# Optimization experiments

Measured on AMD Instinct MI355X. Metric: run time of the kernel, lower is better.

The kernel has to match this reference:

```python
import jax, jax.numpy as jnp
import numpy as np

N_ANCH = 8400      # YOLOv8 anchors for 640x640
NUM_CLS = 600
H_IMG = 640
W_IMG = 640
PRE_NMS = 1024     # fixed pre-NMS pool (replaces dynamic NMS input size)
M_MAX = 31         # fixed max surviving detections (padded)
OUT = 224
SCORE_THRESH = 0.1
IOU_THRESH = 0.45
SCALES = jnp.array([0.7071, 1.0, 1.4142], jnp.float32)
MEAN = jnp.array([0.485, 0.456, 0.406], jnp.float32).reshape(1, 3, 1, 1)
STD = jnp.array([0.229, 0.224, 0.225], jnp.float32).reshape(1, 3, 1, 1)
ALLOWED = [41, 68, 70, 74, 87, 95, 113, 144, 150, 158, 164, 165, 193, 205, 212, 224,
           257, 298, 310, 335, 351, 354, 390, 393, 401, 403, 439, 442, 457, 466, 489,
           510, 512, 514, 524, 530, 531, 543, 546, 554, 565, 573, 580, 587, 588, 591]


def setup_inputs() -> dict:
    key = jax.random.key(0)
    k1, k2, k3, k4 = jax.random.split(key, 4)
    # box channels: cx,cy in pixel coords; w,h in [20, 200] px
    cxcy = jax.random.uniform(k1, (1, 2, N_ANCH), jnp.float32) * jnp.array([W_IMG, H_IMG], jnp.float32).reshape(1, 2, 1)
    wh = jax.random.uniform(k2, (1, 2, N_ANCH), jnp.float32) * 180.0 + 20.0
    logits = jax.random.uniform(k3, (1, NUM_CLS, N_ANCH), jnp.float32)
    raw_pred = jnp.concatenate([cxcy, wh, logits], axis=1)
    image = jax.random.uniform(k4, (1, 3, H_IMG, W_IMG), jnp.float32)
    allowed_cl = jnp.array(ALLOWED, jnp.int32)
    return {"raw_pred": raw_pred, "image": image, "allowed_cl": allowed_cl}


def _pairwise_iou(b):
    # b: [P,4] (x1,y1,x2,y2) -> [P,P] IoU (torchvision convention, no +1)
    area = (b[:, 2] - b[:, 0]) * (b[:, 3] - b[:, 1])
    lt = jnp.maximum(b[:, None, :2], b[None, :, :2])   # [P,P,2]
    rb = jnp.minimum(b[:, None, 2:], b[None, :, 2:])
    wh = jnp.clip(rb - lt, 0.0)
    inter = wh[..., 0] * wh[..., 1]
    union = area[:, None] + area[None, :] - inter
    return inter / jnp.maximum(union, 1e-12)


def _greedy_nms(iou, thr):
    # boxes assumed pre-sorted by descending score
    n = iou.shape[0]
    rng = jnp.arange(n)

    def step(supp, i):
        keep_i = jnp.logical_not(supp[i])
        supp = supp | (keep_i & (iou[i] > thr) & (rng > i))
        return supp, keep_i

    _, keep = jax.lax.scan(step, jnp.zeros(n, bool), rng)
    return keep


def _crop_bilinear(img, box):
    # img: [3,H,W]; box: (x1,y1,x2,y2). roi_align, aligned=True, sampling_ratio=1.
    C, H, W = img.shape
    x1, y1, x2, y2 = box[0], box[1], box[2], box[3]
    bw = (x2 - x1) / OUT
    bh = (y2 - y1) / OUT
    r = jnp.arange(OUT, dtype=jnp.float32) + 0.5
    xs = x1 - 0.5 + r * bw
    ys = y1 - 0.5 + r * bh
    mx = (xs > -1.0) & (xs < W)
    my = (ys > -1.0) & (ys < H)
    xsc = jnp.clip(xs, 0.0, W - 1.0)
    ysc = jnp.clip(ys, 0.0, H - 1.0)
    y0 = jnp.floor(ysc).astype(jnp.int32)
    x0 = jnp.floor(xsc).astype(jnp.int32)
    y1i = jnp.minimum(y0 + 1, H - 1)
    x1i = jnp.minimum(x0 + 1, W - 1)
    wy = ysc - y0.astype(jnp.float32)
    wx = xsc - x0.astype(jnp.float32)
    # separable bilinear: interp rows along y, then columns along x
    rows = img[:, y0, :] * (1.0 - wy)[None, :, None] + img[:, y1i, :] * wy[None, :, None]  # [3,OUT,W]
    out = rows[:, :, x0] * (1.0 - wx)[None, None, :] + rows[:, :, x1i] * wx[None, None, :]  # [3,OUT,OUT]
    return out * (my[None, :, None] & mx[None, None, :]).astype(img.dtype)


def reference(raw_pred, image, allowed_cl):
    x = raw_pred[0].T                            # [N, 4+C]
    cx, cy, w, h = x[:, 0], x[:, 1], x[:, 2], x[:, 3]
    boxes = jnp.stack([cx - w * 0.5, cy - h * 0.5, cx + w * 0.5, cy + h * 0.5], axis=1)
    logits = x[:, 4:]
    scores = logits.max(axis=1)
    classes = logits.argmax(axis=1).astype(jnp.int32)

    # fixed-size pre-NMS pool, sorted by descending score
    sc, idx = jax.lax.top_k(scores, PRE_NMS)
    b = boxes[idx]
    cl = classes[idx]

    keep = _greedy_nms(_pairwise_iou(b), IOU_THRESH)
    in_allowed = (cl[:, None] == allowed_cl[None, :].astype(cl.dtype)).any(axis=1)
    valid = keep & (sc > SCORE_THRESH) & in_allowed

    masked = jnp.where(valid, sc, -jnp.inf)
    topv, topi = jax.lax.top_k(masked, M_MAX)
    sel_valid = topv > -jnp.inf
    sel_boxes = jnp.where(sel_valid[:, None], b[topi], 0.0)
    sel_scores = jnp.where(sel_valid, sc[topi], 0.0)
    sel_cls = jnp.where(sel_valid, cl[topi], 0)

    full_box = jnp.array([[0.0, 0.0, W_IMG - 1.0, H_IMG - 1.0]], jnp.float32)
    final_boxes = jnp.concatenate([full_box, sel_boxes], axis=0)            # [M+1,4]
    final_scores = jnp.concatenate([jnp.ones((1,), jnp.float32), sel_scores])
    final_classes = jnp.concatenate([-jnp.ones((1,), cl.dtype), sel_cls])

    # multi-scale boxes, same center, clamped to image
    bx1, by1, bx2, by2 = (final_boxes[:, i] for i in range(4))
    ccx = (bx1 + bx2) * 0.5
    ccy = (by1 + by2) * 0.5
    ww = (bx2 - bx1)[:, None] * SCALES[None, :] * 0.5
    hh = (by2 - by1)[:, None] * SCALES[None, :] * 0.5
    scaled = jnp.stack([
        jnp.clip(ccx[:, None] - ww, 0.0, W_IMG - 1.0),
        jnp.clip(ccy[:, None] - hh, 0.0, H_IMG - 1.0),
        jnp.clip(ccx[:, None] + ww, 0.0, W_IMG - 1.0),
        jnp.clip(ccy[:, None] + hh, 0.0, H_IMG - 1.0),
    ], axis=-1)                                                             # [M+1,K,4]

    boxes_flat = scaled.reshape(-1, 4)                                      # [(M+1)*K,4]
    crops = jax.vmap(lambda bb: _crop_bilinear(image[0], bb))(boxes_flat)   # [(M+1)*K,3,224,224]
    crops_norm = (crops - MEAN) / STD
    return final_boxes, final_scores, final_classes, crops_norm
```

## Files before the change

### kernel.cpp

```cpp
#include <hip/hip_runtime.h>
#include <hip/hip_bf16.h>
#include <stdint.h>

#define N_ANCH   8400
#define NUM_CLS  600
#define H_IMG    640
#define W_IMG    640
#define PRE_NMS  1024
#define M_MAX    31
#define OUT_SZ   224
#define SCORE_THRESH 0.1f
#define IOU_THRESH   0.45f

__global__ __launch_bounds__(512) void k_prep(
    const float* __restrict__ raw,
    float* __restrict__ x1, float* __restrict__ y1,
    float* __restrict__ x2, float* __restrict__ y2,
    float* __restrict__ sc, int* __restrict__ cls) {
  __shared__ float s_m[8][64];
  __shared__ int   s_mi[8][64];
  const int lane = threadIdx.x & 63;
  const int part = threadIdx.x >> 6;
  const int a = blockIdx.x * 64 + lane;

  float m = -INFINITY; int mi = 0;
  if (a < N_ANCH) {
    const float* lp = raw + (size_t)(4 + part * 75) * N_ANCH + a;
    #pragma unroll 5
    for (int cc = 0; cc < 75; ++cc) {
      float v = lp[(size_t)cc * N_ANCH];
      if (v > m) { m = v; mi = part * 75 + cc; }
    }
  }
  s_m[part][lane] = m; s_mi[part][lane] = mi;
  __syncthreads();
  if (part == 0 && a < N_ANCH) {
    #pragma unroll
    for (int p = 1; p < 8; ++p) {
      float vm = s_m[p][lane];
      if (vm > m) { m = vm; mi = s_mi[p][lane]; }
    }
    sc[a] = m; cls[a] = mi;
    float cx = raw[a];
    float cy = raw[(size_t)1 * N_ANCH + a];
    float w  = raw[(size_t)2 * N_ANCH + a];
    float h  = raw[(size_t)3 * N_ANCH + a];
    x1[a] = cx - w * 0.5f; y1[a] = cy - h * 0.5f;
    x2[a] = cx + w * 0.5f; y2[a] = cy + h * 0.5f;
  }
}

__device__ __forceinline__ unsigned long long shflxor64(unsigned long long v, int j) {
  int lo = __shfl_xor((int)(unsigned int)v, j, 64);
  int hi = __shfl_xor((int)(unsigned int)(v >> 32), j, 64);
  return ((unsigned long long)(unsigned int)hi << 32) | (unsigned int)lo;
}

__global__ __launch_bounds__(1024) void k_select(
    const float* __restrict__ sc, const int* __restrict__ cls,
    const float* __restrict__ x1, const float* __restrict__ y1,
    const float* __restrict__ x2, const float* __restrict__ y2,
    float* __restrict__ t_sc, float* __restrict__ tb, int* __restrict__ t_cl) {
  __shared__ unsigned int hist[8][2048];
  __shared__ unsigned long long C[N_ANCH];
  __shared__ unsigned long long s_sel[PRE_NMS];
  __shared__ unsigned int wt[16];
  __shared__ int s_bstar, s_above, s_cnt;
  __shared__ unsigned long long s_thr;

  const int tid = threadIdx.x;
  const int lane = tid & 63, wid = tid >> 6;
  unsigned int* hf = &hist[0][0];

  unsigned long long ka[9];
  bool kv[9];
  #pragma unroll
  for (int e = 0; e < 9; ++e) {
    int a = tid + e * 1024;
    kv[e] = (a < N_ANCH);
    float s = kv[e] ? sc[a] : 0.0f;
    ka[e] = (((unsigned long long)__float_as_uint(s)) << 32) |
            (unsigned long long)(0xFFFFFFFFu - (unsigned)a);
  }

  int need = PRE_NMS;
  unsigned long long thr = 0ULL;
  int m = 0;

  #pragma unroll
  for (int i = tid; i < 8 * 2048; i += 1024) hf[i] = 0;
  if (tid == 0) s_cnt = 0;
  __syncthreads();
  #pragma unroll
  for (int e = 0; e < 9; ++e)
    if (kv[e]) atomicAdd(&hist[wid & 7][(unsigned)((ka[e] >> 51) & 2047ULL)], 1u);
  __syncthreads();
  {
    unsigned int h0 = 0, h1 = 0;
    #pragma unroll
    for (int cp = 0; cp < 8; ++cp) { h0 += hist[cp][2 * tid]; h1 += hist[cp][2 * tid + 1]; }
    unsigned int suf = h0 + h1;
    #pragma unroll
    for (int o = 1; o < 64; o <<= 1) {
      unsigned int t = __shfl_down(suf, o, 64);
      if (lane + o < 64) suf += t;
    }
    if (lane == 0) wt[wid] = suf;
    __syncthreads();
    unsigned int add = 0;
    #pragma unroll
    for (int q = 0; q < 16; ++q) if (q > wid) add += wt[q];
    const unsigned int S0 = suf + add, S1 = S0 - h0, S2 = S1 - h1;
    if ((int)S0 >= need && (int)S1 < need) { s_bstar = 2 * tid;     s_above = (int)S1; }
    if ((int)S1 >= need && (int)S2 < need) { s_bstar = 2 * tid + 1; s_above = (int)S2; }
  }
  __syncthreads();
  {
    const int bstar = s_bstar;
    need -= s_above;
    thr |= (unsigned long long)bstar << 51;
    #pragma unroll
    for (int e = 0; e < 9; ++e)
      if (kv[e] && (int)((ka[e] >> 51) & 2047ULL) == bstar)
        C[atomicAdd(&s_cnt, 1)] = ka[e];
  }
  __syncthreads();
  m = s_cnt;

  const int shifts[5] = {40, 29, 18, 7, 0};
  for (int si = 0; si < 5 && m > 64; ++si) {
    const int shift = shifts[si];
    unsigned long long cu[9];
    #pragma unroll
    for (int e = 0; e < 9; ++e) {
      int i = tid + e * 1024;
      cu[e] = (i < m) ? C[i] : 0ULL;
    }
    #pragma unroll
    for (int i = tid; i < 8 * 2048; i += 1024) hf[i] = 0;
    if (tid == 0) s_cnt = 0;
    __syncthreads();
    #pragma unroll
    for (int e = 0; e < 9; ++e)
      if (tid + e * 1024 < m)
        atomicAdd(&hist[wid & 7][(unsigned)((cu[e] >> shift) & 2047ULL)], 1u);
    __syncthreads();
    {
      unsigned int h0 = 0, h1 = 0;
      #pragma unroll
      for (int cp = 0; cp < 8; ++cp) { h0 += hist[cp][2 * tid]; h1 += hist[cp][2 * tid + 1]; }
      unsigned int suf = h0 + h1;
      #pragma unroll
      for (int o = 1; o < 64; o <<= 1) {
        unsigned int t = __shfl_down(suf, o, 64);
        if (lane + o < 64) suf += t;
      }
      if (lane == 0) wt[wid] = suf;
      __syncthreads();
      unsigned int add = 0;
      #pragma unroll
      for (int q = 0; q < 16; ++q) if (q > wid) add += wt[q];
      const unsigned int S0 = suf + add, S1 = S0 - h0, S2 = S1 - h1;
      if ((int)S0 >= need && (int)S1 < need) { s_bstar = 2 * tid;     s_above = (int)S1; }
      if ((int)S1 >= need && (int)S2 < need) { s_bstar = 2 * tid + 1; s_above = (int)S2; }
    }
    __syncthreads();
    {
      const int bstar = s_bstar;
      need -= s_above;
      thr |= (unsigned long long)bstar << shift;
      #pragma unroll
      for (int e = 0; e < 9; ++e)
        if (tid + e * 1024 < m && (int)((cu[e] >> shift) & 2047ULL) == bstar)
          C[atomicAdd(&s_cnt, 1)] = cu[e];
    }
    __syncthreads();
    m = s_cnt;
  }

  if (wid == 0) {
    unsigned long long v = (lane < m) ? C[lane] : 0ULL;
    for (int k2 = 2; k2 <= 64; k2 <<= 1) {
      for (int j = k2 >> 1; j > 0; j >>= 1) {
        unsigned long long pv = shflxor64(v, j);
        bool keepmax = (((lane & k2) == 0) == ((lane & j) == 0));
        if (keepmax == (pv > v)) v = pv;
      }
    }
    if (lane == need - 1) s_thr = v;
  }
  if (tid == 0) s_cnt = 0;
  __syncthreads();

  const unsigned long long thrv = s_thr;
  #pragma unroll
  for (int e = 0; e < 9; ++e)
    if (kv[e] && ka[e] >= thrv) {
      int p = atomicAdd(&s_cnt, 1);
      if (p < PRE_NMS) s_sel[p] = ka[e];
    }
  __syncthreads();

  unsigned long long v = s_sel[tid];
  for (int k2 = 2; k2 <= PRE_NMS; k2 <<= 1) {
    for (int j = k2 >> 1; j > 0; j >>= 1) {
      unsigned long long pv;
      if (j >= 64) {
        __syncthreads();
        C[tid] = v;
        __syncthreads();
        pv = C[tid ^ j];
      } else {
        pv = shflxor64(v, j);
      }
      bool keepmax = (((tid & k2) == 0) == ((tid & j) == 0));
      if (keepmax == (pv > v)) v = pv;
    }
  }

  const int idx = (int)(0xFFFFFFFFu - (unsigned)(v & 0xFFFFFFFFULL));
  t_sc[tid] = __uint_as_float((unsigned)(v >> 32));
  tb[tid]               = x1[idx];
  tb[PRE_NMS + tid]     = y1[idx];
  tb[2 * PRE_NMS + tid] = x2[idx];
  tb[3 * PRE_NMS + tid] = y2[idx];
  t_cl[tid] = cls[idx];
}

__global__ __launch_bounds__(256) void k_iou_mask(
    const float* __restrict__ tb, unsigned long long* __restrict__ mask) {
  __shared__ float bx1[PRE_NMS], by1[PRE_NMS], bx2[PRE_NMS], by2[PRE_NMS], bar[PRE_NMS];
  const int tid = threadIdx.x;
  for (int a = tid; a < PRE_NMS; a += 256) {
    float X1 = tb[a], Y1 = tb[PRE_NMS + a], X2 = tb[2 * PRE_NMS + a], Y2 = tb[3 * PRE_NMS + a];
    bx1[a] = X1; by1[a] = Y1; bx2[a] = X2; by2[a] = Y2;
    bar[a] = (X2 - X1) * (Y2 - Y1);
  }
  __syncthreads();
  const int g = blockIdx.x * 256 + tid;
  const int i = g >> 4;
  const int w = g & 15;
  const float ix1 = bx1[i], iy1 = by1[i], ix2 = bx2[i], iy2 = by2[i], ia = bar[i];
  unsigned long long m = 0ULL;
  const int j0 = w * 64;
  #pragma unroll 8
  for (int l = 0; l < 64; ++l) {
    const int jj = (l + 4 * w) & 63;
    const int j = j0 + jj;
    float ltx = fmaxf(ix1, bx1[j]);
    float lty = fmaxf(iy1, by1[j]);
    float rbx = fminf(ix2, bx2[j]);
    float rby = fminf(iy2, by2[j]);
    float ww = fmaxf(rbx - ltx, 0.0f);
    float hh = fmaxf(rby - lty, 0.0f);
    float inter = ww * hh;
    float uni = ia + bar[j] - inter;
    float iou = inter / fmaxf(uni, 1e-12f);
    if (iou > IOU_THRESH && j > i) m |= (1ULL << jj);
  }
  mask[(size_t)i * 16 + w] = m;
}

__device__ __forceinline__ unsigned long long rdlane64(unsigned long long v, int lane) {
  unsigned int lo = (unsigned int)v;
  unsigned int hi = (unsigned int)(v >> 32);
  unsigned int a = (unsigned int)__builtin_amdgcn_readlane((int)lo, lane);
  unsigned int b = (unsigned int)__builtin_amdgcn_readlane((int)hi, lane);
  return ((unsigned long long)b << 32) | (unsigned long long)a;
}

__global__ __launch_bounds__(1024) void k_nms_final(
    const unsigned long long* __restrict__ mask,
    const float* __restrict__ t_sc, const float* __restrict__ tb,
    const int* __restrict__ t_cl, const int* __restrict__ allowed, int n_allowed,
    float* __restrict__ out, float* __restrict__ cropbox) {
  __shared__ unsigned long long L[PRE_NMS * 17];
  __shared__ unsigned long long s_K[16];
  __shared__ unsigned long long s_albm[16];
  __shared__ int s_selr[M_MAX];
  __shared__ int s_nsel;
  const int tid = threadIdx.x;
  const int lane = tid & 63, wid = tid >> 6;

  const ulonglong2* m2 = (const ulonglong2*)mask;
  #pragma unroll
  for (int k = 0; k < 8; ++k) {
    int t2 = tid + k * 1024;
    ulonglong2 val = m2[t2];
    int row = t2 >> 3;
    int w0 = (t2 & 7) * 2;
    L[row * 17 + w0]     = val.x;
    L[row * 17 + w0 + 1] = val.y;
  }
  if (tid < 16) s_albm[tid] = 0ULL;
  __syncthreads();
  if (tid < n_allowed) {
    int c = allowed[tid];
    atomicOr(&s_albm[c >> 6], 1ULL << (c & 63));
  }

  unsigned long long suppw = 0ULL;

  for (int c = 0; c < 16; ++c) {
    if (wid == c) {
      unsigned long long d = L[(c * 64 + lane) * 17 + c];
      unsigned int slo = (unsigned int)__builtin_amdgcn_readfirstlane((int)(unsigned int)suppw);
      unsigned int shi = (unsigned int)__builtin_amdgcn_readfirstlane((int)(unsigned int)(suppw >> 32));
      unsigned long long sup = ((unsigned long long)shi << 32) | slo;
      unsigned long long K = 0ULL;
      #pragma unroll
      for (int i = 0; i < 64; ++i) {
        unsigned long long di = rdlane64(d, i);
        const bool kept = ((sup >> i) & 1ULL) == 0ULL;
        K   |= kept ? (1ULL << i) : 0ULL;
        sup |= kept ? di : 0ULL;
      }
      if (lane == 0) s_K[c] = K;
    }
    __syncthreads();
    {
      unsigned long long Kc = s_K[c];
      unsigned long long v =
          ((Kc >> (unsigned)lane) & 1ULL) ? L[(c * 64 + lane) * 17 + wid] : 0ULL;
      #pragma unroll
      for (int o = 1; o < 64; o <<= 1) v |= shflxor64(v, o);
      suppw |= v;
    }
  }
  __syncthreads();

  if (wid == 0) {
    bool validf[16];
    int cnt = 0;
    #pragma unroll
    for (int k = 0; k < 16; ++k) {
      const int r = lane * 16 + k;
      bool kp = ((s_K[r >> 6] >> (unsigned)(r & 63)) & 1ULL) != 0ULL;
      float s = t_sc[r];
      int c = t_cl[r];
      bool ina = ((s_albm[c >> 6] >> (unsigned)(c & 63)) & 1ULL) != 0ULL;
      bool v = kp && (s > SCORE_THRESH) && ina;
      validf[k] = v;
      cnt += v ? 1 : 0;
    }
    int scan = cnt;
    #pragma unroll
    for (int o = 1; o < 64; o <<= 1) {
      int v = __shfl_up(scan, o, 64);
      if (lane >= o) scan += v;
    }
    const int excl = scan - cnt;
    int rk = excl;
    #pragma unroll
    for (int k = 0; k < 16; ++k) {
      if (validf[k]) {
        if (rk < M_MAX) s_selr[rk] = lane * 16 + k;
        rk++;
      }
    }
    if (lane == 63) s_nsel = (scan < M_MAX) ? scan : M_MAX;
  }
  __syncthreads();

  if (wid == 0 && lane < 32) {
    const int nsel = s_nsel;
    float b0, b1, b2, b3, fsc, fcl;
    if (lane == 0) {
      b0 = 0.0f; b1 = 0.0f; b2 = (float)(W_IMG - 1); b3 = (float)(H_IMG - 1);
      fsc = 1.0f; fcl = -1.0f;
    } else if (lane <= nsel) {
      int r = s_selr[lane - 1];
      b0 = tb[r]; b1 = tb[PRE_NMS + r]; b2 = tb[2 * PRE_NMS + r]; b3 = tb[3 * PRE_NMS + r];
      fsc = t_sc[r]; fcl = (float)t_cl[r];
    } else {
      b0 = b1 = b2 = b3 = 0.0f; fsc = 0.0f; fcl = 0.0f;
    }
    out[lane * 4 + 0] = b0; out[lane * 4 + 1] = b1;
    out[lane * 4 + 2] = b2; out[lane * 4 + 3] = b3;
    out[128 + lane] = fsc;
    out[160 + lane] = fcl;

    const float ccx = (b0 + b2) * 0.5f;
    const float ccy = (b1 + b3) * 0.5f;
    const float bwd = b2 - b0;
    const float bhd = b3 - b1;
    const float scl3[3] = {0.7071f, 1.0f, 1.4142f};
    #pragma unroll
    for (int s3 = 0; s3 < 3; ++s3) {
      float ww = bwd * scl3[s3] * 0.5f;
      float hh = bhd * scl3[s3] * 0.5f;
      float cx1 = fminf(fmaxf(ccx - ww, 0.0f), (float)(W_IMG - 1));
      float cy1 = fminf(fmaxf(ccy - hh, 0.0f), (float)(H_IMG - 1));
      float cx2 = fminf(fmaxf(ccx + ww, 0.0f), (float)(W_IMG - 1));
      float cy2 = fminf(fmaxf(ccy + hh, 0.0f), (float)(H_IMG - 1));
      const int bi = (lane * 3 + s3) * 4;
      cropbox[bi + 0] = cx1; cropbox[bi + 1] = cy1;
      cropbox[bi + 2] = cx2; cropbox[bi + 3] = cy2;
    }
  }
}

__global__ __launch_bounds__(256) void k_crop(
    const float* __restrict__ img, const float* __restrict__ cropbox,
    float* __restrict__ out) {
  const int gid = blockIdx.x * 256 + threadIdx.x;
  const int x4 = gid % (OUT_SZ / 4);
  const int t1 = gid / (OUT_SZ / 4);
  const int py = t1 % OUT_SZ;
  const int t2 = t1 / OUT_SZ;
  const int c = t2 % 3;
  const int b = t2 / 3;
  if (b >= 96) return;

  const float bx1 = cropbox[b * 4 + 0];
  const float by1 = cropbox[b * 4 + 1];
  const float bx2 = cropbox[b * 4 + 2];
  const float by2 = cropbox[b * 4 + 3];
  const float bw = (bx2 - bx1) / (float)OUT_SZ;
  const float bh = (by2 - by1) / (float)OUT_SZ;

  const float ys = by1 - 0.5f + ((float)py + 0.5f) * bh;
  const bool my = (ys > -1.0f) && (ys < (float)H_IMG);
  const float ysc = fminf(fmaxf(ys, 0.0f), (float)(H_IMG - 1));
  const int y0 = (int)floorf(ysc);
  const int y1i = min(y0 + 1, H_IMG - 1);
  const float wy = ysc - (float)y0;

  const float* r0p = img + (size_t)c * (H_IMG * W_IMG) + (size_t)y0 * W_IMG;
  const float* r1p = img + (size_t)c * (H_IMG * W_IMG) + (size_t)y1i * W_IMG;

  const float mean = (c == 0) ? 0.485f : ((c == 1) ? 0.456f : 0.406f);
  const float stdv = (c == 0) ? 0.229f : ((c == 1) ? 0.224f : 0.225f);

  auto pix = [&](int px) -> float {
    const float xs = bx1 - 0.5f + ((float)px + 0.5f) * bw;
    const bool mx = (xs > -1.0f) && (xs < (float)W_IMG);
    const float xsc = fminf(fmaxf(xs, 0.0f), (float)(W_IMG - 1));
    const int x0 = (int)floorf(xsc);
    const int x1i = min(x0 + 1, W_IMG - 1);
    const float wx = xsc - (float)x0;
    const float r0 = r0p[x0] * (1.0f - wy) + r1p[x0] * wy;
    const float r1 = r0p[x1i] * (1.0f - wy) + r1p[x1i] * wy;
    float v = r0 * (1.0f - wx) + r1 * wx;
    v = (mx && my) ? v : 0.0f;
    return (v - mean) / stdv;
  };

  const int pxb = x4 * 4;
  float4 res;
  res.x = pix(pxb + 0);
  res.y = pix(pxb + 1);
  res.z = pix(pxb + 2);
  res.w = pix(pxb + 3);
  reinterpret_cast<float4*>(out)[gid] = res;
}

extern "C" void kernel_launch(void* const* d_in, const int* in_sizes, int n_in,
                              void* d_out, int out_size, void* d_ws, size_t ws_size,
                              hipStream_t stream) {
  const float* raw = (const float*)d_in[0];
  const float* img = (const float*)d_in[1];
  const int* allowed = (const int*)d_in[2];
  float* out = (float*)d_out;

  unsigned long long* mask = (unsigned long long*)d_ws;
  float* fbase = (float*)((char*)d_ws + (size_t)PRE_NMS * 16 * 8);
  float* x1 = fbase + 0 * N_ANCH;
  float* y1 = fbase + 1 * N_ANCH;
  float* x2 = fbase + 2 * N_ANCH;
  float* y2 = fbase + 3 * N_ANCH;
  float* sc = fbase + 4 * N_ANCH;
  int*   cls = (int*)(fbase + 5 * N_ANCH);
  float* t_sc = fbase + 6 * N_ANCH;
  float* tb   = t_sc + PRE_NMS;
  int*   t_cl = (int*)(tb + 4 * PRE_NMS);
  float* cropbox = (float*)(t_cl + PRE_NMS);

  k_prep<<<(N_ANCH + 63) / 64, 512, 0, stream>>>(raw, x1, y1, x2, y2, sc, cls);
  k_select<<<1, 1024, 0, stream>>>(sc, cls, x1, y1, x2, y2, t_sc, tb, t_cl);
  k_iou_mask<<<64, 256, 0, stream>>>(tb, mask);
  k_nms_final<<<1, 1024, 0, stream>>>(mask, t_sc, tb, t_cl, allowed,
                                      in_sizes[2], out, cropbox);
  const int total4 = 96 * 3 * OUT_SZ * OUT_SZ / 4;
  k_crop<<<(total4 + 255) / 256, 256, 0, stream>>>(img, cropbox, out + 192);
}
```

Measured before the change: 130.2 us.

## Transpose IoU mask layout and stream NMS columns from global memory into registers

New measurement: 128.5 us. Within noise of the previous version (-1.3%).

```diff
diff --git a/kernel.cpp b/kernel.cpp
--- a/kernel.cpp
+++ b/kernel.cpp
@@ -228,7 +228,7 @@
 }
 
 __global__ __launch_bounds__(256) void k_iou_mask(
-    const float* __restrict__ tb, unsigned long long* __restrict__ mask) {
+    const float* __restrict__ tb, unsigned long long* __restrict__ maskT) {
   __shared__ float bx1[PRE_NMS], by1[PRE_NMS], bx2[PRE_NMS], by2[PRE_NMS], bar[PRE_NMS];
   const int tid = threadIdx.x;
   for (int a = tid; a < PRE_NMS; a += 256) {
@@ -238,14 +238,13 @@
   }
   __syncthreads();
   const int g = blockIdx.x * 256 + tid;
-  const int i = g >> 4;
-  const int w = g & 15;
+  const int w = g >> 10;
+  const int i = g & 1023;
   const float ix1 = bx1[i], iy1 = by1[i], ix2 = bx2[i], iy2 = by2[i], ia = bar[i];
   unsigned long long m = 0ULL;
   const int j0 = w * 64;
   #pragma unroll 8
-  for (int l = 0; l < 64; ++l) {
-    const int jj = (l + 4 * w) & 63;
+  for (int jj = 0; jj < 64; ++jj) {
     const int j = j0 + jj;
     float ltx = fmaxf(ix1, bx1[j]);
     float lty = fmaxf(iy1, by1[j]);
@@ -258,7 +257,7 @@
     float iou = inter / fmaxf(uni, 1e-12f);
     if (iou > IOU_THRESH && j > i) m |= (1ULL << jj);
   }
-  mask[(size_t)i * 16 + w] = m;
+  maskT[g] = m;
 }
 
 __device__ __forceinline__ unsigned long long rdlane64(unsigned long long v, int lane) {
@@ -270,11 +269,10 @@
 }
 
 __global__ __launch_bounds__(1024) void k_nms_final(
-    const unsigned long long* __restrict__ mask,
+    const unsigned long long* __restrict__ maskT,
     const float* __restrict__ t_sc, const float* __restrict__ tb,
     const int* __restrict__ t_cl, const int* __restrict__ allowed, int n_allowed,
     float* __restrict__ out, float* __restrict__ cropbox) {
-  __shared__ unsigned long long L[PRE_NMS * 17];
   __shared__ unsigned long long s_K[16];
   __shared__ unsigned long long s_albm[16];
   __shared__ int s_selr[M_MAX];
@@ -282,16 +280,6 @@
   const int tid = threadIdx.x;
   const int lane = tid & 63, wid = tid >> 6;
 
-  const ulonglong2* m2 = (const ulonglong2*)mask;
-  #pragma unroll
-  for (int k = 0; k < 8; ++k) {
-    int t2 = tid + k * 1024;
-    ulonglong2 val = m2[t2];
-    int row = t2 >> 3;
-    int w0 = (t2 & 7) * 2;
-    L[row * 17 + w0]     = val.x;
-    L[row * 17 + w0 + 1] = val.y;
-  }
   if (tid < 16) s_albm[tid] = 0ULL;
   __syncthreads();
   if (tid < n_allowed) {
@@ -299,34 +287,50 @@
     atomicOr(&s_albm[c >> 6], 1ULL << (c & 63));
   }
 
+  const unsigned long long* colbase = maskT + (size_t)wid * 1024;
   unsigned long long suppw = 0ULL;
 
-  for (int c = 0; c < 16; ++c) {
-    if (wid == c) {
-      unsigned long long d = L[(c * 64 + lane) * 17 + c];
-      unsigned int slo = (unsigned int)__builtin_amdgcn_readfirstlane((int)(unsigned int)suppw);
-      unsigned int shi = (unsigned int)__builtin_amdgcn_readfirstlane((int)(unsigned int)(suppw >> 32));
-      unsigned long long sup = ((unsigned long long)shi << 32) | slo;
-      unsigned long long K = 0ULL;
-      #pragma unroll
-      for (int i = 0; i < 64; ++i) {
-        unsigned long long di = rdlane64(d, i);
-        const bool kept = ((sup >> i) & 1ULL) == 0ULL;
-        K   |= kept ? (1ULL << i) : 0ULL;
-        sup |= kept ? di : 0ULL;
-      }
-      if (lane == 0) s_K[c] = K;
-    }
-    __syncthreads();
-    {
-      unsigned long long Kc = s_K[c];
-      unsigned long long v =
-          ((Kc >> (unsigned)lane) & 1ULL) ? L[(c * 64 + lane) * 17 + wid] : 0ULL;
-      #pragma unroll
-      for (int o = 1; o < 64; o <<= 1) v |= shflxor64(v, o);
-      suppw |= v;
-    }
-  }
+  unsigned long long rA = colbase[lane];
+  unsigned long long rB = colbase[64 + lane];
+
+#define NMS_STEP(REG, CHUNK)                                                  \
+  {                                                                           \
+    if (wid == (CHUNK)) {                                                     \
+      unsigned int slo = (unsigned int)__builtin_amdgcn_readfirstlane(        \
+          (int)(unsigned int)suppw);                                          \
+      unsigned int shi = (unsigned int)__builtin_amdgcn_readfirstlane(        \
+          (int)(unsigned int)(suppw >> 32));                                  \
+      unsigned long long sup = ((unsigned long long)shi << 32) | slo;         \
+      unsigned long long K = 0ULL;                                            \
+      _Pragma("unroll")                                                       \
+      for (int i = 0; i < 64; ++i) {                                          \
+        unsigned long long di = rdlane64((REG), i);                           \
+        const bool kept = ((sup >> i) & 1ULL) == 0ULL;                        \
+        K   |= kept ? (1ULL << i) : 0ULL;                                     \
+        sup |= kept ? di : 0ULL;                                              \
+      }                                                                       \
+      if (lane == 0) s_K[(CHUNK)] = K;                                        \
+    }                                                                         \
+    __syncthreads();                                                          \
+    {                                                                         \
+      unsigned long long Kc = s_K[(CHUNK)];                                   \
+      unsigned long long v =                                                  \
+          ((Kc >> (unsigned)lane) & 1ULL) ? (REG) : 0ULL;                     \
+      _Pragma("unroll")                                                       \
+      for (int o = 1; o < 64; o <<= 1) v |= shflxor64(v, o);                  \
+      suppw |= v;                                                             \
+    }                                                                         \
+  }
+
+  #pragma unroll 1
+  for (int c = 0; c < 16; c += 2) {
+    unsigned long long nA = (c + 2 < 16) ? colbase[(c + 2) * 64 + lane] : 0ULL;
+    NMS_STEP(rA, c)
+    unsigned long long nB = (c + 3 < 16) ? colbase[(c + 3) * 64 + lane] : 0ULL;
+    NMS_STEP(rB, c + 1)
+    rA = nA; rB = nB;
+  }
+#undef NMS_STEP
   __syncthreads();
 
   if (wid == 0) {
@@ -463,7 +467,7 @@
   const int* allowed = (const int*)d_in[2];
   float* out = (float*)d_out;
 
-  unsigned long long* mask = (unsigned long long*)d_ws;
+  unsigned long long* maskT = (unsigned long long*)d_ws;
   float* fbase = (float*)((char*)d_ws + (size_t)PRE_NMS * 16 * 8);
   float* x1 = fbase + 0 * N_ANCH;
   float* y1 = fbase + 1 * N_ANCH;
@@ -478,8 +482,8 @@
 
   k_prep<<<(N_ANCH + 63) / 64, 512, 0, stream>>>(raw, x1, y1, x2, y2, sc, cls);
   k_select<<<1, 1024, 0, stream>>>(sc, cls, x1, y1, x2, y2, t_sc, tb, t_cl);
-  k_iou_mask<<<64, 256, 0, stream>>>(tb, mask);
-  k_nms_final<<<1, 1024, 0, stream>>>(mask, t_sc, tb, t_cl, allowed,
+  k_iou_mask<<<64, 256, 0, stream>>>(tb, maskT);
+  k_nms_final<<<1, 1024, 0, stream>>>(maskT, t_sc, tb, t_cl, allowed,
                                       in_sizes[2], out, cropbox);
   const int total4 = 96 * 3 * OUT_SZ * OUT_SZ / 4;
   k_crop<<<(total4 + 255) / 256, 256, 0, stream>>>(img, cropbox, out + 192);
```

## Fuse IoU mask computation into single-block NMS kernel with triangular work balance

Applied to the files above, without the earlier changes.

Measured after the change: 227.7 us. +74.8%, slower.

```diff
diff --git a/kernel.cpp b/kernel.cpp
--- a/kernel.cpp
+++ b/kernel.cpp
@@ -227,40 +227,6 @@
   t_cl[tid] = cls[idx];
 }
 
-__global__ __launch_bounds__(256) void k_iou_mask(
-    const float* __restrict__ tb, unsigned long long* __restrict__ mask) {
-  __shared__ float bx1[PRE_NMS], by1[PRE_NMS], bx2[PRE_NMS], by2[PRE_NMS], bar[PRE_NMS];
-  const int tid = threadIdx.x;
-  for (int a = tid; a < PRE_NMS; a += 256) {
-    float X1 = tb[a], Y1 = tb[PRE_NMS + a], X2 = tb[2 * PRE_NMS + a], Y2 = tb[3 * PRE_NMS + a];
-    bx1[a] = X1; by1[a] = Y1; bx2[a] = X2; by2[a] = Y2;
-    bar[a] = (X2 - X1) * (Y2 - Y1);
-  }
-  __syncthreads();
-  const int g = blockIdx.x * 256 + tid;
-  const int i = g >> 4;
-  const int w = g & 15;
-  const float ix1 = bx1[i], iy1 = by1[i], ix2 = bx2[i], iy2 = by2[i], ia = bar[i];
-  unsigned long long m = 0ULL;
-  const int j0 = w * 64;
-  #pragma unroll 8
-  for (int l = 0; l < 64; ++l) {
-    const int jj = (l + 4 * w) & 63;
-    const int j = j0 + jj;
-    float ltx = fmaxf(ix1, bx1[j]);
-    float lty = fmaxf(iy1, by1[j]);
-    float rbx = fminf(ix2, bx2[j]);
-    float rby = fminf(iy2, by2[j]);
-    float ww = fmaxf(rbx - ltx, 0.0f);
-    float hh = fmaxf(rby - lty, 0.0f);
-    float inter = ww * hh;
-    float uni = ia + bar[j] - inter;
-    float iou = inter / fmaxf(uni, 1e-12f);
-    if (iou > IOU_THRESH && j > i) m |= (1ULL << jj);
-  }
-  mask[(size_t)i * 16 + w] = m;
-}
-
 __device__ __forceinline__ unsigned long long rdlane64(unsigned long long v, int lane) {
   unsigned int lo = (unsigned int)v;
   unsigned int hi = (unsigned int)(v >> 32);
@@ -269,12 +235,12 @@
   return ((unsigned long long)b << 32) | (unsigned long long)a;
 }
 
-__global__ __launch_bounds__(1024) void k_nms_final(
-    const unsigned long long* __restrict__ mask,
+__global__ __launch_bounds__(1024) void k_iou_nms(
     const float* __restrict__ t_sc, const float* __restrict__ tb,
     const int* __restrict__ t_cl, const int* __restrict__ allowed, int n_allowed,
     float* __restrict__ out, float* __restrict__ cropbox) {
-  __shared__ unsigned long long L[PRE_NMS * 17];
+  __shared__ unsigned long long L[16 * PRE_NMS];
+  __shared__ float bx1[PRE_NMS], by1[PRE_NMS], bx2[PRE_NMS], by2[PRE_NMS], bar[PRE_NMS];
   __shared__ unsigned long long s_K[16];
   __shared__ unsigned long long s_albm[16];
   __shared__ int s_selr[M_MAX];
@@ -282,15 +248,11 @@
   const int tid = threadIdx.x;
   const int lane = tid & 63, wid = tid >> 6;
 
-  const ulonglong2* m2 = (const ulonglong2*)mask;
-  #pragma unroll
-  for (int k = 0; k < 8; ++k) {
-    int t2 = tid + k * 1024;
-    ulonglong2 val = m2[t2];
-    int row = t2 >> 3;
-    int w0 = (t2 & 7) * 2;
-    L[row * 17 + w0]     = val.x;
-    L[row * 17 + w0 + 1] = val.y;
+  {
+    float X1 = tb[tid], Y1 = tb[PRE_NMS + tid];
+    float X2 = tb[2 * PRE_NMS + tid], Y2 = tb[3 * PRE_NMS + tid];
+    bx1[tid] = X1; by1[tid] = Y1; bx2[tid] = X2; by2[tid] = Y2;
+    bar[tid] = (X2 - X1) * (Y2 - Y1);
   }
   if (tid < 16) s_albm[tid] = 0ULL;
   __syncthreads();
@@ -299,11 +261,40 @@
     atomicOr(&s_albm[c >> 6], 1ULL << (c & 63));
   }
 
+  {
+    const int g = wid >> 2, r = wid & 3;
+    const int q = (g == 0) ? r : (g == 1) ? (15 - r) : (g == 2) ? (4 + r) : (11 - r);
+    const int i = q * 64 + lane;
+    const float ix1 = bx1[i], iy1 = by1[i], ix2 = bx2[i], iy2 = by2[i], ia = bar[i];
+    for (int k = 0; k < 16; ++k) {
+      unsigned long long m = 0ULL;
+      if (k >= q) {
+        const int j0 = k * 64;
+        #pragma unroll 8
+        for (int jj = 0; jj < 64; ++jj) {
+          const int j = j0 + jj;
+          float ltx = fmaxf(ix1, bx1[j]);
+          float lty = fmaxf(iy1, by1[j]);
+          float rbx = fminf(ix2, bx2[j]);
+          float rby = fminf(iy2, by2[j]);
+          float ww = fmaxf(rbx - ltx, 0.0f);
+          float hh = fmaxf(rby - lty, 0.0f);
+          float inter = ww * hh;
+          float uni = ia + bar[j] - inter;
+          float iou = inter / fmaxf(uni, 1e-12f);
+          if (iou > IOU_THRESH && j > i) m |= (1ULL << jj);
+        }
+      }
+      L[k * PRE_NMS + i] = m;
+    }
+  }
+  __syncthreads();
+
   unsigned long long suppw = 0ULL;
-
+  #pragma unroll 1
   for (int c = 0; c < 16; ++c) {
     if (wid == c) {
-      unsigned long long d = L[(c * 64 + lane) * 17 + c];
+      unsigned long long d = L[c * PRE_NMS + c * 64 + lane];
       unsigned int slo = (unsigned int)__builtin_amdgcn_readfirstlane((int)(unsigned int)suppw);
       unsigned int shi = (unsigned int)__builtin_amdgcn_readfirstlane((int)(unsigned int)(suppw >> 32));
       unsigned long long sup = ((unsigned long long)shi << 32) | slo;
@@ -321,7 +312,7 @@
     {
       unsigned long long Kc = s_K[c];
       unsigned long long v =
-          ((Kc >> (unsigned)lane) & 1ULL) ? L[(c * 64 + lane) * 17 + wid] : 0ULL;
+          ((Kc >> (unsigned)lane) & 1ULL) ? L[wid * PRE_NMS + c * 64 + lane] : 0ULL;
       #pragma unroll
       for (int o = 1; o < 64; o <<= 1) v |= shflxor64(v, o);
       suppw |= v;
@@ -370,7 +361,7 @@
       fsc = 1.0f; fcl = -1.0f;
     } else if (lane <= nsel) {
       int r = s_selr[lane - 1];
-      b0 = tb[r]; b1 = tb[PRE_NMS + r]; b2 = tb[2 * PRE_NMS + r]; b3 = tb[3 * PRE_NMS + r];
+      b0 = bx1[r]; b1 = by1[r]; b2 = bx2[r]; b3 = by2[r];
       fsc = t_sc[r]; fcl = (float)t_cl[r];
     } else {
       b0 = b1 = b2 = b3 = 0.0f; fsc = 0.0f; fcl = 0.0f;
@@ -463,7 +454,6 @@
   const int* allowed = (const int*)d_in[2];
   float* out = (float*)d_out;
 
-  unsigned long long* mask = (unsigned long long*)d_ws;
   float* fbase = (float*)((char*)d_ws + (size_t)PRE_NMS * 16 * 8);
   float* x1 = fbase + 0 * N_ANCH;
   float* y1 = fbase + 1 * N_ANCH;
@@ -478,9 +468,8 @@
 
   k_prep<<<(N_ANCH + 63) / 64, 512, 0, stream>>>(raw, x1, y1, x2, y2, sc, cls);
   k_select<<<1, 1024, 0, stream>>>(sc, cls, x1, y1, x2, y2, t_sc, tb, t_cl);
-  k_iou_mask<<<64, 256, 0, stream>>>(tb, mask);
-  k_nms_final<<<1, 1024, 0, stream>>>(mask, t_sc, tb, t_cl, allowed,
-                                      in_sizes[2], out, cropbox);
+  k_iou_nms<<<1, 1024, 0, stream>>>(t_sc, tb, t_cl, allowed,
+                                    in_sizes[2], out, cropbox);
   const int total4 = 96 * 3 * OUT_SZ * OUT_SZ / 4;
   k_crop<<<(total4 + 255) / 256, 256, 0, stream>>>(img, cropbox, out + 192);
 }
```
